# Optimization experiments

Hardware: AMD Instinct MI355X
Metric: run time of the kernel (lower is better)

Reference implementation:

```python
import jax, jax.numpy as jnp
import numpy as np

N = 16384
IN_F = 128
PSI_F = 16
OUT_F = 128


def setup_inputs() -> dict:
    key = jax.random.key(0)
    ks = jax.random.split(key, 10)
    nodes = jax.random.normal(ks[0], (N, IN_F), dtype=jnp.float32)
    adjacency = jax.random.randint(ks[1], (N, N), 0, 2, dtype=jnp.int32)
    psi_w1 = jax.random.normal(ks[2], (IN_F, 15), dtype=jnp.float32) * (1.0 / np.sqrt(IN_F))
    psi_b1 = jax.random.normal(ks[3], (15,), dtype=jnp.float32) * 0.01
    psi_w2 = jax.random.normal(ks[4], (15, PSI_F), dtype=jnp.float32) * (1.0 / np.sqrt(15.0))
    psi_b2 = jax.random.normal(ks[5], (PSI_F,), dtype=jnp.float32) * 0.01
    fi_w1 = jax.random.normal(ks[6], (IN_F + PSI_F, 25), dtype=jnp.float32) * (1.0 / np.sqrt(IN_F + PSI_F))
    fi_b1 = jax.random.normal(ks[7], (25,), dtype=jnp.float32) * 0.01
    fi_w2 = jax.random.normal(ks[8], (25, OUT_F), dtype=jnp.float32) * (1.0 / np.sqrt(25.0))
    fi_b2 = jax.random.normal(ks[9], (OUT_F,), dtype=jnp.float32) * 0.01
    return {"nodes": nodes, "adjacency": adjacency,
            "psi_w1": psi_w1, "psi_b1": psi_b1, "psi_w2": psi_w2, "psi_b2": psi_b2,
            "fi_w1": fi_w1, "fi_b1": fi_b1, "fi_w2": fi_w2, "fi_b2": fi_b2}


def reference(nodes, adjacency, psi_w1, psi_b1, psi_w2, psi_b2, fi_w1, fi_b1, fi_w2, fi_b2):
    A = adjacency.astype(nodes.dtype)            # [N, N], 0/1
    c = jnp.sum(A, axis=0)                        # [N] neighbor counts (column sums)
    # psi MLP applied per node once (equivalent to per-neighbor application)
    h = jax.nn.relu(nodes @ psi_w1 + psi_b1)      # [N, 15]
    h = jax.nn.relu(h @ psi_w2 + psi_b2)          # [N, PSI_F]
    # mean aggregation over in-neighbors: psi_out[i] = sum_j A[j,i]*h[j] / c[i]
    psi_out = (A.T @ h) / c[:, None]              # [N, PSI_F]
    z = jnp.concatenate([nodes, psi_out], axis=1) # [N, IN_F+PSI_F]
    g = jax.nn.relu(z @ fi_w1 + fi_b1)            # [N, 25]
    return jax.nn.relu(g @ fi_w2 + fi_b2)         # [N, OUT_F]
```

## Files before the change

### kernel.cpp

```cpp
#include <hip/hip_runtime.h>

#define N_NODES 16384
#define IN_F    128
#define H1      15
#define PSI_F   16
#define ZF      (IN_F + PSI_F)
#define H2      25
#define OUT_F   128

#define AGG_TB   256
#define AGG_CPT  4
#define AGG_CPB  (AGG_TB * AGG_CPT)
#define AGG_CB   (N_NODES / AGG_CPB)
#define AGG_RS   64
#define AGG_RPB  (N_NODES / AGG_RS)

typedef int   v4i __attribute__((ext_vector_type(4)));
typedef float v4f __attribute__((ext_vector_type(4)));

__global__ __launch_bounds__(64) void psi_kernel(
    const float* __restrict__ nodes,
    const float* __restrict__ w1, const float* __restrict__ b1,
    const float* __restrict__ w2, const float* __restrict__ b2,
    float* __restrict__ h) {
  __shared__ float sw1[IN_F * 16];
  __shared__ float sw2[16 * PSI_F];
  __shared__ float sb1[16];
  __shared__ float sb2[PSI_F];
  const int t = threadIdx.x;
  for (int i = t; i < IN_F * 16; i += 64) {
    int k = i >> 4, j = i & 15;
    sw1[i] = (j < H1) ? w1[k * H1 + j] : 0.0f;
  }
  for (int i = t; i < 16 * PSI_F; i += 64) {
    int j = i >> 4, j2 = i & 15;
    sw2[i] = (j < H1) ? w2[j * PSI_F + j2] : 0.0f;
  }
  if (t < 16)   sb1[t] = (t < H1) ? b1[t] : 0.0f;
  if (t < PSI_F) sb2[t] = b2[t];
  __syncthreads();

  const int node = blockIdx.x * 64 + t;
  const float4* __restrict__ row = (const float4*)(nodes + (size_t)node * IN_F);
  const float4* __restrict__ sw1v = (const float4*)sw1;
  const float4* __restrict__ sw2v = (const float4*)sw2;

  float a1[16];
#pragma unroll
  for (int j = 0; j < 16; ++j) a1[j] = sb1[j];

#pragma unroll 4
  for (int k4 = 0; k4 < IN_F / 4; ++k4) {
    float4 x = row[k4];
    float xs[4] = {x.x, x.y, x.z, x.w};
#pragma unroll
    for (int kk = 0; kk < 4; ++kk) {
#pragma unroll
      for (int j4 = 0; j4 < 4; ++j4) {
        float4 w = sw1v[(k4 * 4 + kk) * 4 + j4];
        a1[j4 * 4 + 0] = fmaf(xs[kk], w.x, a1[j4 * 4 + 0]);
        a1[j4 * 4 + 1] = fmaf(xs[kk], w.y, a1[j4 * 4 + 1]);
        a1[j4 * 4 + 2] = fmaf(xs[kk], w.z, a1[j4 * 4 + 2]);
        a1[j4 * 4 + 3] = fmaf(xs[kk], w.w, a1[j4 * 4 + 3]);
      }
    }
  }

  float a2[PSI_F];
#pragma unroll
  for (int j2 = 0; j2 < PSI_F; ++j2) a2[j2] = sb2[j2];
#pragma unroll
  for (int j = 0; j < 16; ++j) {
    float v = fmaxf(a1[j], 0.0f);
#pragma unroll
    for (int j4 = 0; j4 < 4; ++j4) {
      float4 w = sw2v[j * 4 + j4];
      a2[j4 * 4 + 0] = fmaf(v, w.x, a2[j4 * 4 + 0]);
      a2[j4 * 4 + 1] = fmaf(v, w.y, a2[j4 * 4 + 1]);
      a2[j4 * 4 + 2] = fmaf(v, w.z, a2[j4 * 4 + 2]);
      a2[j4 * 4 + 3] = fmaf(v, w.w, a2[j4 * 4 + 3]);
    }
  }

  float4* __restrict__ hp = (float4*)(h + (size_t)node * PSI_F);
#pragma unroll
  for (int j4 = 0; j4 < 4; ++j4) {
    hp[j4] = make_float4(fmaxf(a2[j4 * 4 + 0], 0.0f), fmaxf(a2[j4 * 4 + 1], 0.0f),
                         fmaxf(a2[j4 * 4 + 2], 0.0f), fmaxf(a2[j4 * 4 + 3], 0.0f));
  }
}

__global__ __launch_bounds__(256) void agg_kernel(
    const int* __restrict__ A, const float* __restrict__ h,
    float* __restrict__ pacc, float* __restrict__ pcnt) {
  __shared__ float sh[AGG_RPB * PSI_F];
  const int cb = blockIdx.x % AGG_CB;
  const int rs = blockIdx.x / AGG_CB;
  const int r0 = rs * AGG_RPB;

  {
    const float4* __restrict__ hsrc = (const float4*)(h + (size_t)r0 * PSI_F);
    float4* __restrict__ shv = (float4*)sh;
    for (int i = threadIdx.x; i < AGG_RPB * PSI_F / 4; i += AGG_TB) shv[i] = hsrc[i];
  }
  __syncthreads();

  const int c0 = cb * AGG_CPB + threadIdx.x * AGG_CPT;

  float s[AGG_CPT][PSI_F];
  float n[AGG_CPT];
#pragma unroll
  for (int c = 0; c < AGG_CPT; ++c) {
    n[c] = 0.0f;
#pragma unroll
    for (int k = 0; k < PSI_F; ++k) s[c][k] = 0.0f;
  }

  const v4i* __restrict__ ap = (const v4i*)(A + (size_t)r0 * N_NODES + c0);
  const float4* __restrict__ shv = (const float4*)sh;

#pragma unroll 4
  for (int r = 0; r < AGG_RPB; ++r) {
    v4i av = __builtin_nontemporal_load(ap);
    ap += N_NODES / 4;
    float a[AGG_CPT] = {(float)av[0], (float)av[1], (float)av[2], (float)av[3]};
    float4 hv[4] = {shv[r * 4 + 0], shv[r * 4 + 1], shv[r * 4 + 2], shv[r * 4 + 3]};
#pragma unroll
    for (int c = 0; c < AGG_CPT; ++c) {
#pragma unroll
      for (int q = 0; q < 4; ++q) {
        s[c][q * 4 + 0] = fmaf(a[c], hv[q].x, s[c][q * 4 + 0]);
        s[c][q * 4 + 1] = fmaf(a[c], hv[q].y, s[c][q * 4 + 1]);
        s[c][q * 4 + 2] = fmaf(a[c], hv[q].z, s[c][q * 4 + 2]);
        s[c][q * 4 + 3] = fmaf(a[c], hv[q].w, s[c][q * 4 + 3]);
      }
      n[c] += a[c];
    }
  }

  float* __restrict__ pa = pacc + ((size_t)rs * N_NODES + c0) * PSI_F;
#pragma unroll
  for (int c = 0; c < AGG_CPT; ++c) {
#pragma unroll
    for (int q = 0; q < 4; ++q) {
      v4f v = {s[c][q * 4 + 0], s[c][q * 4 + 1], s[c][q * 4 + 2], s[c][q * 4 + 3]};
      __builtin_nontemporal_store(v, (v4f*)(pa + c * PSI_F + q * 4));
    }
  }
  v4f nv = {n[0], n[1], n[2], n[3]};
  __builtin_nontemporal_store(nv, (v4f*)(pcnt + (size_t)rs * N_NODES + c0));
}

__global__ __launch_bounds__(256) void reduce_kernel(
    const float* __restrict__ pacc, const float* __restrict__ pcnt,
    float* __restrict__ acc, float* __restrict__ cnt) {
  const int idx = blockIdx.x * 256 + threadIdx.x;
  float s = 0.0f;
  const float* __restrict__ p = pacc + idx;
#pragma unroll 8
  for (int rs = 0; rs < AGG_RS; ++rs) {
    s += *p;
    p += (size_t)N_NODES * PSI_F;
  }
  acc[idx] = s;
  if (idx < N_NODES) {
    float c = 0.0f;
    const float* __restrict__ q = pcnt + idx;
#pragma unroll 8
    for (int rs = 0; rs < AGG_RS; ++rs) {
      c += *q;
      q += N_NODES;
    }
    cnt[idx] = c;
  }
}

__global__ __launch_bounds__(64) void fi_kernel(
    const float* __restrict__ nodes, const float* __restrict__ acc, const float* __restrict__ cnt,
    const float* __restrict__ w1, const float* __restrict__ b1,
    const float* __restrict__ w2, const float* __restrict__ b2,
    float* __restrict__ out) {
  __shared__ float sw1[ZF * 28];
  __shared__ float sw2[H2 * OUT_F];
  __shared__ float sb1[28];
  __shared__ float sb2[OUT_F];
  const int t = threadIdx.x;
  for (int i = t; i < ZF * 28; i += 64) {
    int k = i / 28, j = i % 28;
    sw1[i] = (j < H2) ? w1[k * H2 + j] : 0.0f;
  }
  for (int i = t; i < H2 * OUT_F; i += 64) sw2[i] = w2[i];
  if (t < 28) sb1[t] = (t < H2) ? b1[t] : 0.0f;
  for (int i = t; i < OUT_F; i += 64) sb2[i] = b2[i];
  __syncthreads();

  const int node = blockIdx.x * 64 + t;
  const float4* __restrict__ sw1v = (const float4*)sw1;
  const float4* __restrict__ sw2v = (const float4*)sw2;

  float g[28];
#pragma unroll
  for (int j = 0; j < 28; ++j) g[j] = sb1[j];

  const float4* __restrict__ nrow = (const float4*)(nodes + (size_t)node * IN_F);
#pragma unroll 2
  for (int k4 = 0; k4 < IN_F / 4; ++k4) {
    float4 x = nrow[k4];
    float xs[4] = {x.x, x.y, x.z, x.w};
#pragma unroll
    for (int kk = 0; kk < 4; ++kk) {
      const int k = k4 * 4 + kk;
#pragma unroll
      for (int j4 = 0; j4 < 7; ++j4) {
        float4 w = sw1v[k * 7 + j4];
        g[j4 * 4 + 0] = fmaf(xs[kk], w.x, g[j4 * 4 + 0]);
        g[j4 * 4 + 1] = fmaf(xs[kk], w.y, g[j4 * 4 + 1]);
        g[j4 * 4 + 2] = fmaf(xs[kk], w.z, g[j4 * 4 + 2]);
        g[j4 * 4 + 3] = fmaf(xs[kk], w.w, g[j4 * 4 + 3]);
      }
    }
  }

  const float invc = 1.0f / cnt[node];
  const float4* __restrict__ prow = (const float4*)(acc + (size_t)node * PSI_F);
#pragma unroll
  for (int k4 = 0; k4 < PSI_F / 4; ++k4) {
    float4 p = prow[k4];
    float xs[4] = {p.x * invc, p.y * invc, p.z * invc, p.w * invc};
#pragma unroll
    for (int kk = 0; kk < 4; ++kk) {
      const int k = IN_F + k4 * 4 + kk;
#pragma unroll
      for (int j4 = 0; j4 < 7; ++j4) {
        float4 w = sw1v[k * 7 + j4];
        g[j4 * 4 + 0] = fmaf(xs[kk], w.x, g[j4 * 4 + 0]);
        g[j4 * 4 + 1] = fmaf(xs[kk], w.y, g[j4 * 4 + 1]);
        g[j4 * 4 + 2] = fmaf(xs[kk], w.z, g[j4 * 4 + 2]);
        g[j4 * 4 + 3] = fmaf(xs[kk], w.w, g[j4 * 4 + 3]);
      }
    }
  }

#pragma unroll
  for (int j = 0; j < H2; ++j) g[j] = fmaxf(g[j], 0.0f);

  float4* __restrict__ op = (float4*)(out + (size_t)node * OUT_F);
#pragma unroll
  for (int oc = 0; oc < 4; ++oc) {
    float o[32];
#pragma unroll
    for (int i = 0; i < 32; ++i) o[i] = sb2[oc * 32 + i];
#pragma unroll
    for (int j = 0; j < H2; ++j) {
      float gv = g[j];
#pragma unroll
      for (int o4 = 0; o4 < 8; ++o4) {
        float4 w = sw2v[(j * OUT_F + oc * 32) / 4 + o4];
        o[o4 * 4 + 0] = fmaf(gv, w.x, o[o4 * 4 + 0]);
        o[o4 * 4 + 1] = fmaf(gv, w.y, o[o4 * 4 + 1]);
        o[o4 * 4 + 2] = fmaf(gv, w.z, o[o4 * 4 + 2]);
        o[o4 * 4 + 3] = fmaf(gv, w.w, o[o4 * 4 + 3]);
      }
    }
#pragma unroll
    for (int o4 = 0; o4 < 8; ++o4) {
      op[oc * 8 + o4] = make_float4(fmaxf(o[o4 * 4 + 0], 0.0f), fmaxf(o[o4 * 4 + 1], 0.0f),
                                    fmaxf(o[o4 * 4 + 2], 0.0f), fmaxf(o[o4 * 4 + 3], 0.0f));
    }
  }
}

extern "C" void kernel_launch(void* const* d_in, const int* in_sizes, int n_in,
                              void* d_out, int out_size, void* d_ws, size_t ws_size,
                              hipStream_t stream) {
  const float* nodes  = (const float*)d_in[0];
  const int*   A      = (const int*)d_in[1];
  const float* psi_w1 = (const float*)d_in[2];
  const float* psi_b1 = (const float*)d_in[3];
  const float* psi_w2 = (const float*)d_in[4];
  const float* psi_b2 = (const float*)d_in[5];
  const float* fi_w1  = (const float*)d_in[6];
  const float* fi_b1  = (const float*)d_in[7];
  const float* fi_w2  = (const float*)d_in[8];
  const float* fi_b2  = (const float*)d_in[9];
  float* out = (float*)d_out;

  float* h    = (float*)d_ws;
  float* pacc = h + (size_t)N_NODES * PSI_F;
  float* pcnt = pacc + (size_t)AGG_RS * N_NODES * PSI_F;
  float* acc  = pcnt + (size_t)AGG_RS * N_NODES;
  float* cnt  = acc + (size_t)N_NODES * PSI_F;

  psi_kernel<<<N_NODES / 64, 64, 0, stream>>>(nodes, psi_w1, psi_b1, psi_w2, psi_b2, h);
  agg_kernel<<<AGG_CB * AGG_RS, AGG_TB, 0, stream>>>(A, h, pacc, pcnt);
  reduce_kernel<<<N_NODES * PSI_F / 256, 256, 0, stream>>>(pacc, pcnt, acc, cnt);
  fi_kernel<<<N_NODES / 64, 64, 0, stream>>>(nodes, acc, cnt, fi_w1, fi_b1, fi_w2, fi_b2, out);
}
```

Before: 1.504 ms.

## Fuse partial-sum reduction into fi kernel and halve row splits in aggregation

```diff
diff --git a/kernel.cpp b/kernel.cpp
--- a/kernel.cpp
+++ b/kernel.cpp
@@ -12,7 +12,7 @@
 #define AGG_CPT  4
 #define AGG_CPB  (AGG_TB * AGG_CPT)
 #define AGG_CB   (N_NODES / AGG_CPB)
-#define AGG_RS   64
+#define AGG_RS   32
 #define AGG_RPB  (N_NODES / AGG_RS)
 
 typedef int   v4i __attribute__((ext_vector_type(4)));
@@ -101,7 +101,9 @@
   {
     const float4* __restrict__ hsrc = (const float4*)(h + (size_t)r0 * PSI_F);
     float4* __restrict__ shv = (float4*)sh;
-    for (int i = threadIdx.x; i < AGG_RPB * PSI_F / 4; i += AGG_TB) shv[i] = hsrc[i];
+#pragma unroll
+    for (int i = 0; i < AGG_RPB * PSI_F / 4 / AGG_TB; ++i)
+      shv[i * AGG_TB + threadIdx.x] = hsrc[i * AGG_TB + threadIdx.x];
   }
   __syncthreads();
 
@@ -119,7 +121,7 @@
   const v4i* __restrict__ ap = (const v4i*)(A + (size_t)r0 * N_NODES + c0);
   const float4* __restrict__ shv = (const float4*)sh;
 
-#pragma unroll 4
+#pragma unroll 8
   for (int r = 0; r < AGG_RPB; ++r) {
     v4i av = __builtin_nontemporal_load(ap);
     ap += N_NODES / 4;
@@ -151,32 +153,9 @@
   __builtin_nontemporal_store(nv, (v4f*)(pcnt + (size_t)rs * N_NODES + c0));
 }
 
-__global__ __launch_bounds__(256) void reduce_kernel(
+__global__ __launch_bounds__(64) void fi_kernel(
+    const float* __restrict__ nodes,
     const float* __restrict__ pacc, const float* __restrict__ pcnt,
-    float* __restrict__ acc, float* __restrict__ cnt) {
-  const int idx = blockIdx.x * 256 + threadIdx.x;
-  float s = 0.0f;
-  const float* __restrict__ p = pacc + idx;
-#pragma unroll 8
-  for (int rs = 0; rs < AGG_RS; ++rs) {
-    s += *p;
-    p += (size_t)N_NODES * PSI_F;
-  }
-  acc[idx] = s;
-  if (idx < N_NODES) {
-    float c = 0.0f;
-    const float* __restrict__ q = pcnt + idx;
-#pragma unroll 8
-    for (int rs = 0; rs < AGG_RS; ++rs) {
-      c += *q;
-      q += N_NODES;
-    }
-    cnt[idx] = c;
-  }
-}
-
-__global__ __launch_bounds__(64) void fi_kernel(
-    const float* __restrict__ nodes, const float* __restrict__ acc, const float* __restrict__ cnt,
     const float* __restrict__ w1, const float* __restrict__ b1,
     const float* __restrict__ w2, const float* __restrict__ b2,
     float* __restrict__ out) {
@@ -198,6 +177,24 @@
   const float4* __restrict__ sw1v = (const float4*)sw1;
   const float4* __restrict__ sw2v = (const float4*)sw2;
 
+  float ps[PSI_F];
+#pragma unroll
+  for (int k = 0; k < PSI_F; ++k) ps[k] = 0.0f;
+  float cn = 0.0f;
+#pragma unroll 4
+  for (int rs = 0; rs < AGG_RS; ++rs) {
+    const float4* __restrict__ pp =
+        (const float4*)(pacc + ((size_t)rs * N_NODES + node) * PSI_F);
+#pragma unroll
+    for (int q = 0; q < 4; ++q) {
+      float4 p = pp[q];
+      ps[q * 4 + 0] += p.x; ps[q * 4 + 1] += p.y;
+      ps[q * 4 + 2] += p.z; ps[q * 4 + 3] += p.w;
+    }
+    cn += pcnt[(size_t)rs * N_NODES + node];
+  }
+  const float invc = 1.0f / cn;
+
   float g[28];
 #pragma unroll
   for (int j = 0; j < 28; ++j) g[j] = sb1[j];
@@ -221,23 +218,17 @@
     }
   }
 
-  const float invc = 1.0f / cnt[node];
-  const float4* __restrict__ prow = (const float4*)(acc + (size_t)node * PSI_F);
-#pragma unroll
-  for (int k4 = 0; k4 < PSI_F / 4; ++k4) {
-    float4 p = prow[k4];
-    float xs[4] = {p.x * invc, p.y * invc, p.z * invc, p.w * invc};
-#pragma unroll
-    for (int kk = 0; kk < 4; ++kk) {
-      const int k = IN_F + k4 * 4 + kk;
-#pragma unroll
-      for (int j4 = 0; j4 < 7; ++j4) {
-        float4 w = sw1v[k * 7 + j4];
-        g[j4 * 4 + 0] = fmaf(xs[kk], w.x, g[j4 * 4 + 0]);
-        g[j4 * 4 + 1] = fmaf(xs[kk], w.y, g[j4 * 4 + 1]);
-        g[j4 * 4 + 2] = fmaf(xs[kk], w.z, g[j4 * 4 + 2]);
-        g[j4 * 4 + 3] = fmaf(xs[kk], w.w, g[j4 * 4 + 3]);
-      }
+#pragma unroll
+  for (int kk = 0; kk < PSI_F; ++kk) {
+    const float xv = ps[kk] * invc;
+    const int k = IN_F + kk;
+#pragma unroll
+    for (int j4 = 0; j4 < 7; ++j4) {
+      float4 w = sw1v[k * 7 + j4];
+      g[j4 * 4 + 0] = fmaf(xv, w.x, g[j4 * 4 + 0]);
+      g[j4 * 4 + 1] = fmaf(xv, w.y, g[j4 * 4 + 1]);
+      g[j4 * 4 + 2] = fmaf(xv, w.z, g[j4 * 4 + 2]);
+      g[j4 * 4 + 3] = fmaf(xv, w.w, g[j4 * 4 + 3]);
     }
   }
 
@@ -288,11 +279,8 @@
   float* h    = (float*)d_ws;
   float* pacc = h + (size_t)N_NODES * PSI_F;
   float* pcnt = pacc + (size_t)AGG_RS * N_NODES * PSI_F;
-  float* acc  = pcnt + (size_t)AGG_RS * N_NODES;
-  float* cnt  = acc + (size_t)N_NODES * PSI_F;
 
   psi_kernel<<<N_NODES / 64, 64, 0, stream>>>(nodes, psi_w1, psi_b1, psi_w2, psi_b2, h);
   agg_kernel<<<AGG_CB * AGG_RS, AGG_TB, 0, stream>>>(A, h, pacc, pcnt);
-  reduce_kernel<<<N_NODES * PSI_F / 256, 256, 0, stream>>>(pacc, pcnt, acc, cnt);
-  fi_kernel<<<N_NODES / 64, 64, 0, stream>>>(nodes, acc, cnt, fi_w1, fi_b1, fi_w2, fi_b2, out);
-}
+  fi_kernel<<<N_NODES / 64, 64, 0, stream>>>(nodes, pacc, pcnt, fi_w1, fi_b1, fi_w2, fi_b2, out);
+}
```

Measured after the change: 1.418 ms. -5.7%, faster.
